# Performance work log

Hardware: AMD Instinct MI355X
Metric: run time of the kernel (lower is better)

Reference implementation:

```python
import jax, jax.numpy as jnp
import numpy as np

N = 20000      # n_nodes
E = 320000     # n_edges (multiple of 4, so _from_coo drops nothing)
D = 512        # embed_dim
H = 8          # num_heads
DK = D // H    # d_k = 64


def setup_inputs() -> dict:
    key = jax.random.key(0)
    ks = jax.random.split(key, 12)
    x = jax.random.normal(ks[0], (N, D), jnp.float32)
    rows = jnp.sort(jax.random.randint(ks[1], (E,), 0, N))
    cols = jax.random.randint(ks[2], (E,), 0, N)
    edge_index = jnp.stack([rows, cols]).astype(jnp.int32)  # [2, E]
    att_bias = jax.random.normal(ks[3], (E, H), jnp.float32)
    s = float(1.0 / np.sqrt(D))  # ~xavier scale
    Wq = jax.random.normal(ks[4], (D, D), jnp.float32) * s
    Wk = jax.random.normal(ks[5], (D, D), jnp.float32) * s
    Wv = jax.random.normal(ks[6], (D, D), jnp.float32) * s
    Wo = jax.random.normal(ks[7], (D, D), jnp.float32) * s
    bq = jnp.zeros((D,), jnp.float32)
    bk = jnp.zeros((D,), jnp.float32)
    bv = jnp.zeros((D,), jnp.float32)
    bo = jnp.zeros((D,), jnp.float32)
    return dict(x=x, edge_index=edge_index, att_bias=att_bias,
                Wq=Wq, bq=bq, Wk=Wk, bk=bk, Wv=Wv, bv=bv, Wo=Wo, bo=bo)


def reference(x, edge_index, att_bias, Wq, bq, Wk, bk, Wv, bv, Wo, bo):
    n = x.shape[0]
    rows, cols = edge_index[0], edge_index[1]
    # per-head projections: [n, H, DK]
    q = (x @ Wq + bq).reshape(n, H, DK)
    k = (x @ Wk + bk).reshape(n, H, DK)
    v = (x @ Wv + bv).reshape(n, H, DK)
    scale = 1.0 / jnp.sqrt(jnp.asarray(DK, x.dtype))
    # masked QK^T on the edge pattern, plus additive bias: [E, H]
    logits = jnp.einsum('ehd,ehd->eh', q[rows] * scale, k[cols]) + att_bias
    # CSR (segment) softmax over each destination row
    row_max = jax.ops.segment_max(logits, rows, num_segments=n)      # [n, H]
    p = jnp.exp(logits - row_max[rows])                              # [E, H]
    denom = jax.ops.segment_sum(p, rows, num_segments=n)            # [n, H]
    att = p / denom[rows]                                            # [E, H]
    # sparse-dense bmm: y[i] = sum_{e: rows[e]=i} att[e] * v[cols[e]]
    y = jax.ops.segment_sum(att[:, :, None] * v[cols], rows, num_segments=n)  # [n, H, DK]
    out = y.reshape(n, H * DK) @ Wo + bo
    return out
```

## Files before the change

kernel.cpp:

```cpp
#include <hip/hip_runtime.h>
#include <hip/hip_bf16.h>

typedef unsigned short ushort_t;
typedef unsigned int uint32;
typedef __attribute__((ext_vector_type(8))) short short8;
typedef __attribute__((ext_vector_type(4))) float floatx4;

#define DEV __device__ __forceinline__

#if defined(__has_builtin)
#if __has_builtin(__builtin_amdgcn_sdot4)
#define HAS_SDOT 1
#endif
#endif
#ifndef HAS_SDOT
#define HAS_SDOT 0
#endif

DEV float b2f(ushort_t u) { return __uint_as_float(((uint32)u) << 16); }
DEV ushort_t f2b(float f) {
  __hip_bfloat16 h = __float2bfloat16(f);
  return __builtin_bit_cast(unsigned short, h);
}
DEV void unpack8(const uint4& u, float* f) {
  f[0] = __uint_as_float(u.x << 16); f[1] = __uint_as_float(u.x & 0xffff0000u);
  f[2] = __uint_as_float(u.y << 16); f[3] = __uint_as_float(u.y & 0xffff0000u);
  f[4] = __uint_as_float(u.z << 16); f[5] = __uint_as_float(u.z & 0xffff0000u);
  f[6] = __uint_as_float(u.w << 16); f[7] = __uint_as_float(u.w & 0xffff0000u);
}
DEV void unpack_i8x8(uint2 u, float* f) {
  f[0] = (float)((int)(u.x << 24) >> 24);
  f[1] = (float)((int)(u.x << 16) >> 24);
  f[2] = (float)((int)(u.x << 8) >> 24);
  f[3] = (float)((int)u.x >> 24);
  f[4] = (float)((int)(u.y << 24) >> 24);
  f[5] = (float)((int)(u.y << 16) >> 24);
  f[6] = (float)((int)(u.y << 8) >> 24);
  f[7] = (float)((int)u.y >> 24);
}

#define GLOAD_LDS(gp, lp) \
  __builtin_amdgcn_global_load_lds((const __attribute__((address_space(1))) uint32*)(gp), \
                                   (__attribute__((address_space(3))) uint32*)(lp), 16, 0, 0)

#define KVROW 1088

__global__ __launch_bounds__(256) void k_detect(const ushort_t* __restrict__ x,
                                                int* __restrict__ flag) {
  __shared__ int red[256];
  int tid = threadIdx.x;
  int wild = 0;
  for (int i = tid; i < 4096; i += 256) {
    uint32 e = (x[i] >> 7) & 0xFFu;
    if (e < 100u || e > 140u) wild++;
  }
  red[tid] = wild;
  __syncthreads();
  for (int s = 128; s > 0; s >>= 1) {
    if (tid < s) red[tid] += red[tid + s];
    __syncthreads();
  }
  if (tid == 0) flag[0] = (red[0] > 400) ? 1 : 0;
}

__global__ __launch_bounds__(256) void k_transpose(
    const void* __restrict__ Wq, const void* __restrict__ Wk,
    const void* __restrict__ Wv, const void* __restrict__ Wo,
    ushort_t* __restrict__ WT4, const int* __restrict__ flagp) {
  __shared__ ushort_t t[32][33];
  int isf32 = *flagp;
  int z = blockIdx.z;
  const void* src = (z == 0) ? Wq : (z == 1) ? Wk : (z == 2) ? Wv : Wo;
  ushort_t* dst = WT4 + (size_t)z * 512 * 512;
  int bx = blockIdx.x, by = blockIdx.y;
  int tx = threadIdx.x, ty = threadIdx.y;
#pragma unroll
  for (int i = 0; i < 4; i++) {
    size_t idx = (size_t)(by * 32 + ty + 8 * i) * 512 + bx * 32 + tx;
    ushort_t v = isf32 ? f2b(((const float*)src)[idx]) : ((const ushort_t*)src)[idx];
    t[ty + 8 * i][tx] = v;
  }
  __syncthreads();
#pragma unroll
  for (int i = 0; i < 4; i++)
    dst[(size_t)(bx * 32 + ty + 8 * i) * 512 + by * 32 + tx] = t[tx][ty + 8 * i];
}

__global__ __launch_bounds__(256) void k_biases(
    const void* __restrict__ bq, const void* __restrict__ bk,
    const void* __restrict__ bv, const void* __restrict__ bo,
    float* __restrict__ biasf, const int* __restrict__ flagp) {
  int i = blockIdx.x * 256 + threadIdx.x;
  if (i >= 2048) return;
  int z = i >> 9, j = i & 511;
  const void* b = (z == 0) ? bq : (z == 1) ? bk : (z == 2) ? bv : bo;
  biasf[i] = (*flagp) ? ((const float*)b)[j] : b2f(((const ushort_t*)b)[j]);
}

__global__ __launch_bounds__(256) void k_convx(
    const void* __restrict__ x, ushort_t* __restrict__ xb, int n8,
    const int* __restrict__ flagp) {
  int i = blockIdx.x * 256 + threadIdx.x;
  if (i >= n8) return;
  if (*flagp) {
    const float* xf = (const float*)x + (size_t)i * 8;
    float4 f0 = ((const float4*)xf)[0];
    float4 f1 = ((const float4*)xf)[1];
    uint4 o;
    o.x = (uint32)f2b(f0.x) | ((uint32)f2b(f0.y) << 16);
    o.y = (uint32)f2b(f0.z) | ((uint32)f2b(f0.w) << 16);
    o.z = (uint32)f2b(f1.x) | ((uint32)f2b(f1.y) << 16);
    o.w = (uint32)f2b(f1.z) | ((uint32)f2b(f1.w) << 16);
    ((uint4*)xb)[i] = o;
  } else {
    ((uint4*)xb)[i] = ((const uint4*)x)[i];
  }
}

__global__ __launch_bounds__(256) void k_convab(
    const void* __restrict__ ab, float* __restrict__ ABc, int n4,
    const int* __restrict__ flagp) {
  if (*flagp) return;
  int i = blockIdx.x * 256 + threadIdx.x;
  if (i >= n4) return;
  uint2 u = ((const uint2*)ab)[i];
  float4 o;
  o.x = __uint_as_float(u.x << 16);
  o.y = __uint_as_float(u.x & 0xffff0000u);
  o.z = __uint_as_float(u.y << 16);
  o.w = __uint_as_float(u.y & 0xffff0000u);
  ((float4*)ABc)[i] = o;
}

__global__ void k_build_rp(const int* __restrict__ rows, int E, int N, int* __restrict__ rp) {
  int i = blockIdx.x * blockDim.x + threadIdx.x;
  if (i > N) return;
  int lo = 0, hi = E;
  while (lo < hi) {
    int mid = (lo + hi) >> 1;
    if (rows[mid] < i) lo = mid + 1; else hi = mid;
  }
  rp[i] = lo;
}

DEV void gemm_body(const ushort_t* __restrict__ A, const ushort_t* __restrict__ BT,
                   const float* __restrict__ bias, void* C,
                   int M, int ldc, float scale, int row0, int by, int mode) {
  __shared__ ushort_t As[2][128 * 32];
  __shared__ ushort_t Bs[2][128 * 32];
  int tid = threadIdx.x;
  int w = tid >> 6, lane = tid & 63;
  int sr = lane >> 2;
  int skz = (((lane & 3) ^ ((lane >> 3) & 3)) * 8);

  floatx4 acc[4][4];
#pragma unroll
  for (int i = 0; i < 4; i++)
#pragma unroll
    for (int j = 0; j < 4; j++)
#pragma unroll
      for (int r = 0; r < 4; r++) acc[i][j][r] = 0.f;

  int lm = lane & 15, quad = lane >> 4;
  int wr = w >> 1, wc = w & 1;
  const int nG = by * 128 + w * 32;

  int rA0 = row0 + w * 32 + sr; if (rA0 >= M) rA0 = M - 1;
  int rA1 = rA0 + 16;          if (rA1 >= M) rA1 = M - 1;
  const ushort_t* gA0 = A + (size_t)rA0 * 512 + skz;
  const ushort_t* gA1 = A + (size_t)rA1 * 512 + skz;
  const ushort_t* gB0 = BT + (size_t)(nG + sr) * 512 + skz;
  const ushort_t* gB1 = BT + (size_t)(nG + 16 + sr) * 512 + skz;

  auto stage = [&](int buf, int k0) {
    GLOAD_LDS(gA0 + k0, &As[buf][(w * 32 + 0) * 32]);
    GLOAD_LDS(gA1 + k0, &As[buf][(w * 32 + 16) * 32]);
    GLOAD_LDS(gB0 + k0, &Bs[buf][(w * 32 + 0) * 32]);
    GLOAD_LDS(gB1 + k0, &Bs[buf][(w * 32 + 16) * 32]);
  };

  int rchunk = (quad ^ ((lm >> 1) & 3)) * 8;

  stage(0, 0);
  __syncthreads();

  for (int ks = 0; ks < 16; ++ks) {
    int cur = ks & 1;
    if (ks < 15) stage(cur ^ 1, (ks + 1) * 32);

    const ushort_t* pa = &As[cur][(wr * 64 + lm) * 32] + rchunk;
    const ushort_t* pb = &Bs[cur][(wc * 64 + lm) * 32] + rchunk;
    short8 af[4], bfr[4];
#pragma unroll
    for (int t4 = 0; t4 < 4; t4++) {
      af[t4]  = *(const short8*)(pa + t4 * 16 * 32);
      bfr[t4] = *(const short8*)(pb + t4 * 16 * 32);
    }
#pragma unroll
    for (int mt = 0; mt < 4; mt++)
#pragma unroll
      for (int nt = 0; nt < 4; nt++)
        acc[mt][nt] = __builtin_amdgcn_mfma_f32_16x16x32_bf16(af[mt], bfr[nt], acc[mt][nt], 0, 0, 0);

    __syncthreads();
  }

  int colB = by * 128 + wc * 64 + lm;
  float bv4[4];
#pragma unroll
  for (int nt = 0; nt < 4; nt++) bv4[nt] = bias[colB + nt * 16];

  if (mode <= 1) {
#pragma unroll
    for (int mt = 0; mt < 4; mt++) {
      int rg0 = row0 + wr * 64 + mt * 16 + quad * 4;
#pragma unroll
      for (int nt = 0; nt < 4; nt++) {
#pragma unroll
        for (int r = 0; r < 4; r++) {
          int rg = rg0 + r;
          if (rg < M) {
            float val = (acc[mt][nt][r] + bv4[nt]) * scale;
            size_t off = (size_t)rg * ldc + colB + nt * 16;
            if (mode == 1) ((float*)C)[off] = val;
            else           ((ushort_t*)C)[off] = f2b(val);
          }
        }
      }
    }
  } else {
    int vslot = (mode == 4);
    int colbase = by * 128 + wc * 64;
    int head = colbase >> 6;
#pragma unroll
    for (int mt = 0; mt < 4; mt++) {
#pragma unroll
      for (int r = 0; r < 4; r++) {
        int rg = row0 + wr * 64 + mt * 16 + quad * 4 + r;
        float v0 = acc[mt][0][r] + bv4[0];
        float v1 = acc[mt][1][r] + bv4[1];
        float v2 = acc[mt][2][r] + bv4[2];
        float v3 = acc[mt][3][r] + bv4[3];
        float am = fmaxf(fmaxf(fabsf(v0), fabsf(v1)), fmaxf(fabsf(v2), fabsf(v3)));
        am = fmaxf(am, __shfl_xor(am, 1));
        am = fmaxf(am, __shfl_xor(am, 2));
        am = fmaxf(am, __shfl_xor(am, 4));
        am = fmaxf(am, __shfl_xor(am, 8));
        am = fmaxf(am, 1e-20f);
        float inv8 = 127.0f / am;
        float sc8 = am * (1.0f / 127.0f);
        if (rg < M) {
          unsigned char* Crow = (unsigned char*)C + (size_t)rg * KVROW;
          unsigned char* bp = Crow + 2 * colbase + 16 * (lm >> 3) + 8 * vslot + (lm & 7);
          bp[ 0] = (unsigned char)(signed char)(int)rintf(v0 * inv8);
          bp[32] = (unsigned char)(signed char)(int)rintf(v1 * inv8);
          bp[64] = (unsigned char)(signed char)(int)rintf(v2 * inv8);
          bp[96] = (unsigned char)(signed char)(int)rintf(v3 * inv8);
          if (lm == 0)
            *(float*)(Crow + 1024 + head * 8 + vslot * 4) = sc8;
        }
      }
    }
  }
}

__global__ __launch_bounds__(256) void k_gemm_qkv(
    const ushort_t* __restrict__ xb, const ushort_t* __restrict__ WT4,
    const float* __restrict__ biasf, ushort_t* Qp, unsigned char* KV8, int M) {
  int z = blockIdx.z;
  const ushort_t* BT = WT4 + (size_t)z * 512 * 512;
  const float* bias = biasf + (size_t)z * 512;
  if (z == 0)
    gemm_body(xb, BT, bias, Qp, M, 512, 0.125f, blockIdx.x * 128, blockIdx.y, 0);
  else
    gemm_body(xb, BT, bias, KV8, M, 0, 1.0f, blockIdx.x * 128, blockIdx.y, z == 1 ? 3 : 4);
}

__global__ __launch_bounds__(256) void k_gemm_out(
    const ushort_t* __restrict__ y, const ushort_t* __restrict__ WT4,
    const float* __restrict__ biasf, void* out, int M,
    const int* __restrict__ flagp) {
  gemm_body(y, WT4 + (size_t)3 * 512 * 512, biasf + 3 * 512, out, M, 512, 1.0f,
            blockIdx.x * 128, blockIdx.y, *flagp);
}

__global__ __launch_bounds__(256) void k_edge(
    ushort_t* Qy, const unsigned char* __restrict__ KV8,
    const void* __restrict__ ab, const float* __restrict__ ABc,
    const int* __restrict__ cols, const int* __restrict__ rp, int Nn,
    const int* __restrict__ flagp) {
  int node = blockIdx.x * 4 + (threadIdx.x >> 6);
  if (node >= Nn) return;
  int lane = threadIdx.x & 63;
  int h8 = lane >> 3;
  const float* abf32 = (*flagp) ? (const float*)ab : ABc;

  uint4 qu = ((const uint4*)(Qy + (size_t)node * 512))[lane];
  float qf[8];
  unpack8(qu, qf);

#if HAS_SDOT
  float qa = 0.f;
#pragma unroll
  for (int j = 0; j < 8; j++) qa = fmaxf(qa, fabsf(qf[j]));
  qa = fmaxf(qa, __shfl_xor(qa, 1));
  qa = fmaxf(qa, __shfl_xor(qa, 2));
  qa = fmaxf(qa, __shfl_xor(qa, 4));
  qa = fmaxf(qa, 1e-20f);
  float qs = qa * (1.0f / 127.0f);
  float qinv = 127.0f / qa;
  int qp0 = 0, qp1 = 0;
#pragma unroll
  for (int j = 0; j < 4; j++) qp0 |= (((int)rintf(qf[j] * qinv)) & 0xFF) << (8 * j);
#pragma unroll
  for (int j = 4; j < 8; j++) qp1 |= (((int)rintf(qf[j] * qinv)) & 0xFF) << (8 * (j - 4));
#endif

  int e0 = rp[node], e1 = rp[node + 1];
  int cnt = e1 - e0;

  float s0 = 0.f, s1 = 0.f;
  float acc0[8], acc1[8];
#pragma unroll
  for (int j = 0; j < 8; j++) { acc0[j] = 0.f; acc1[j] = 0.f; }

  uint4 kvb[4];
  float2 scb[4];
  float abv[4];

  for (int base = 0; base < cnt; base += 64) {
    int rem = cnt - base; if (rem > 64) rem = 64;
    int li = (lane < rem) ? lane : (rem - 1);
    int myc = cols[e0 + base + li];
    const float* abp = abf32 + (size_t)(e0 + base) * 8 + h8;

    auto pref = [&](int t, int slot) {
      int valid = t < rem;
      int c = __builtin_amdgcn_readlane(myc, valid ? t : 0);
      const unsigned char* kvrow = KV8 + (size_t)c * KVROW;
      kvb[slot] = *(const uint4*)(kvrow + lane * 16);
      scb[slot] = *(const float2*)(kvrow + 1024 + h8 * 8);
      float a = abp[(valid ? t : 0) * 8];
      abv[slot] = valid ? a : -1e30f;
    };
    auto consume = [&](int slot, float* acc, float& s) {
#if HAS_SDOT
      int di = __builtin_amdgcn_sdot4(qp0, (int)kvb[slot].x, 0, false);
      di = __builtin_amdgcn_sdot4(qp1, (int)kvb[slot].y, di, false);
      di += __shfl_xor(di, 1);
      di += __shfl_xor(di, 2);
      di += __shfl_xor(di, 4);
      float logit = fminf(fmaf((float)di * qs, scb[slot].x, abv[slot]), 80.f);
#else
      float kf[8];
      uint2 ku; ku.x = kvb[slot].x; ku.y = kvb[slot].y;
      unpack_i8x8(ku, kf);
      float d = 0.f;
#pragma unroll
      for (int j = 0; j < 8; j++) d = fmaf(qf[j], kf[j], d);
      d += __shfl_xor(d, 1);
      d += __shfl_xor(d, 2);
      d += __shfl_xor(d, 4);
      float logit = fminf(fmaf(d, scb[slot].x, abv[slot]), 80.f);
#endif
      float pw = __expf(logit);
      s += pw;
      float pwv = pw * scb[slot].y;
      float vf[8];
      uint2 vu; vu.x = kvb[slot].z; vu.y = kvb[slot].w;
      unpack_i8x8(vu, vf);
#pragma unroll
      for (int j = 0; j < 8; j++) acc[j] = fmaf(pwv, vf[j], acc[j]);
    };

    pref(0, 0); pref(1, 1); pref(2, 2); pref(3, 3);
    int iters = (rem + 3) >> 2;
    for (int it = 0; it < iters; ++it) {
      int nt = it * 4 + 4;
      consume(0, acc0, s0); pref(nt + 0, 0);
      consume(1, acc1, s1); pref(nt + 1, 1);
      consume(2, acc0, s0); pref(nt + 2, 2);
      consume(3, acc1, s1); pref(nt + 3, 3);
    }
  }

  float s = s0 + s1;
  float inv = (cnt > 0 && s > 0.f) ? 1.f / s : 0.f;
  ushort_t hb[8];
#pragma unroll
  for (int j = 0; j < 8; j++) hb[j] = f2b((acc0[j] + acc1[j]) * inv);
  uint4 uh;
  uh.x = (uint32)hb[0] | ((uint32)hb[1] << 16);
  uh.y = (uint32)hb[2] | ((uint32)hb[3] << 16);
  uh.z = (uint32)hb[4] | ((uint32)hb[5] << 16);
  uh.w = (uint32)hb[6] | ((uint32)hb[7] << 16);
  ((uint4*)(Qy + (size_t)node * 512))[lane] = uh;
}

extern "C" void kernel_launch(void* const* d_in, const int* in_sizes, int n_in,
                              void* d_out, int out_size, void* d_ws, size_t ws_size,
                              hipStream_t stream) {
  const void* x  = d_in[0];
  const int* ei  = (const int*)d_in[1];
  const void* ab = d_in[2];
  const void* Wq = d_in[3];
  const void* bq = d_in[4];
  const void* Wk = d_in[5];
  const void* bk = d_in[6];
  const void* Wv = d_in[7];
  const void* bv = d_in[8];
  const void* Wo = d_in[9];
  const void* bo = d_in[10];

  const int D = 512;
  int M = in_sizes[0] / D;
  int E = in_sizes[1] / 2;
  const int* rows = ei;
  const int* cols = ei + E;

  char* p = (char*)d_ws;
  size_t off = 0;
  auto carve = [&](size_t bytes) -> void* {
    off = (off + 255) & ~(size_t)255;
    void* r = p + off;
    off += bytes;
    return r;
  };
  int* flag          = (int*)carve(4);
  ushort_t* WT4      = (ushort_t*)carve((size_t)4 * 512 * 512 * 2);
  float* biasf       = (float*)carve((size_t)4 * 512 * 4);
  ushort_t* xb       = (ushort_t*)carve((size_t)M * 512 * 2);
  ushort_t* Qp       = (ushort_t*)carve((size_t)M * 512 * 2);
  unsigned char* KV8 = (unsigned char*)carve((size_t)M * KVROW);
  int* rp            = (int*)carve((size_t)(M + 1) * 4);
  (void)ws_size;
  float* ABc = (float*)xb;

  k_detect<<<1, 256, 0, stream>>>((const ushort_t*)x, flag);
  k_transpose<<<dim3(16, 16, 4), dim3(32, 8), 0, stream>>>(Wq, Wk, Wv, Wo, WT4, flag);
  k_biases<<<8, 256, 0, stream>>>(bq, bk, bv, bo, biasf, flag);
  int n8 = M * 512 / 8;
  k_convx<<<(n8 + 255) / 256, 256, 0, stream>>>(x, xb, n8, flag);
  k_build_rp<<<(M + 1 + 255) / 256, 256, 0, stream>>>(rows, E, M, rp);

  int rb = (M + 127) / 128;
  k_gemm_qkv<<<dim3(rb, 4, 3), 256, 0, stream>>>(xb, WT4, biasf, Qp, KV8, M);
  int n4 = E * 8 / 4;
  k_convab<<<(n4 + 255) / 256, 256, 0, stream>>>(ab, ABc, n4, flag);
  k_edge<<<(M + 3) / 4, 256, 0, stream>>>(Qp, KV8, ab, ABc, cols, rp, M, flag);
  k_gemm_out<<<dim3(rb, 4, 1), 256, 0, stream>>>(Qp, WT4, biasf, d_out, M, flag);
}
```

Measured before the change: 274.8 us.

## Pipeline GEMM K-loop with explicit waitcnt barriers and XCD-aware block swizzle

Restructures the GEMM K-loop so the next tile's global-to-LDS load is issued before waiting, using partial vmcnt waits and raw s_barrier instead of __syncthreads, and peels the final iteration. Both GEMM launches are flattened to 1D grids with an XCD-aware remap, so blocks sharing the same row of x/y land on the same chiplet and its L2. The aim is to overlap memory with MFMA work and improve L2 reuse. The hand-written waitcnt counts assume exactly four outstanding loads per stage, which is fragile if the compiler reorders memory operations.

```diff
diff --git a/kernel.cpp b/kernel.cpp
--- a/kernel.cpp
+++ b/kernel.cpp
@@ -44,6 +44,12 @@
                                    (__attribute__((address_space(3))) uint32*)(lp), 16, 0, 0)
 
 #define KVROW 1088
+
+DEV int xcd_swz(int wg, int nwg) {
+  int q = nwg >> 3, r = nwg & 7;
+  int xcd = wg & 7, idx = wg >> 3;
+  return (xcd < r ? xcd * (q + 1) : r * (q + 1) + (xcd - r) * q) + idx;
+}
 
 __global__ __launch_bounds__(256) void k_detect(const ushort_t* __restrict__ x,
                                                 int* __restrict__ flag) {
@@ -181,13 +187,7 @@
 
   int rchunk = (quad ^ ((lm >> 1) & 3)) * 8;
 
-  stage(0, 0);
-  __syncthreads();
-
-  for (int ks = 0; ks < 16; ++ks) {
-    int cur = ks & 1;
-    if (ks < 15) stage(cur ^ 1, (ks + 1) * 32);
-
+  auto compute = [&](int cur) {
     const ushort_t* pa = &As[cur][(wr * 64 + lm) * 32] + rchunk;
     const ushort_t* pb = &Bs[cur][(wc * 64 + lm) * 32] + rchunk;
     short8 af[4], bfr[4];
@@ -201,9 +201,21 @@
 #pragma unroll
       for (int nt = 0; nt < 4; nt++)
         acc[mt][nt] = __builtin_amdgcn_mfma_f32_16x16x32_bf16(af[mt], bfr[nt], acc[mt][nt], 0, 0, 0);
-
-    __syncthreads();
-  }
+  };
+
+  stage(0, 0);
+  for (int ks = 0; ks < 15; ++ks) {
+    int cur = ks & 1;
+    stage(cur ^ 1, (ks + 1) * 32);
+    asm volatile("s_waitcnt vmcnt(4)" ::: "memory");
+    __builtin_amdgcn_s_barrier();
+    compute(cur);
+    asm volatile("s_waitcnt lgkmcnt(0)" ::: "memory");
+    __builtin_amdgcn_s_barrier();
+  }
+  asm volatile("s_waitcnt vmcnt(0)" ::: "memory");
+  __builtin_amdgcn_s_barrier();
+  compute(1);
 
   int colB = by * 128 + wc * 64 + lm;
   float bv4[4];
@@ -267,21 +279,26 @@
 __global__ __launch_bounds__(256) void k_gemm_qkv(
     const ushort_t* __restrict__ xb, const ushort_t* __restrict__ WT4,
     const float* __restrict__ biasf, ushort_t* Qp, unsigned char* KV8, int M) {
-  int z = blockIdx.z;
+  int swz = xcd_swz(blockIdx.x, gridDim.x);
+  int row = swz / 12;
+  int sub = swz - row * 12;
+  int by = sub & 3, z = sub >> 2;
   const ushort_t* BT = WT4 + (size_t)z * 512 * 512;
   const float* bias = biasf + (size_t)z * 512;
   if (z == 0)
-    gemm_body(xb, BT, bias, Qp, M, 512, 0.125f, blockIdx.x * 128, blockIdx.y, 0);
+    gemm_body(xb, BT, bias, Qp, M, 512, 0.125f, row * 128, by, 0);
   else
-    gemm_body(xb, BT, bias, KV8, M, 0, 1.0f, blockIdx.x * 128, blockIdx.y, z == 1 ? 3 : 4);
+    gemm_body(xb, BT, bias, KV8, M, 0, 1.0f, row * 128, by, z == 1 ? 3 : 4);
 }
 
 __global__ __launch_bounds__(256) void k_gemm_out(
     const ushort_t* __restrict__ y, const ushort_t* __restrict__ WT4,
     const float* __restrict__ biasf, void* out, int M,
     const int* __restrict__ flagp) {
+  int swz = xcd_swz(blockIdx.x, gridDim.x);
+  int row = swz >> 2, by = swz & 3;
   gemm_body(y, WT4 + (size_t)3 * 512 * 512, biasf + 3 * 512, out, M, 512, 1.0f,
-            blockIdx.x * 128, blockIdx.y, *flagp);
+            row * 128, by, *flagp);
 }
 
 __global__ __launch_bounds__(256) void k_edge(
@@ -444,9 +461,9 @@
   k_build_rp<<<(M + 1 + 255) / 256, 256, 0, stream>>>(rows, E, M, rp);
 
   int rb = (M + 127) / 128;
-  k_gemm_qkv<<<dim3(rb, 4, 3), 256, 0, stream>>>(xb, WT4, biasf, Qp, KV8, M);
+  k_gemm_qkv<<<rb * 12, 256, 0, stream>>>(xb, WT4, biasf, Qp, KV8, M);
   int n4 = E * 8 / 4;
   k_convab<<<(n4 + 255) / 256, 256, 0, stream>>>(ab, ABc, n4, flag);
   k_edge<<<(M + 3) / 4, 256, 0, stream>>>(Qp, KV8, ab, ABc, cols, rp, M, flag);
-  k_gemm_out<<<dim3(rb, 4, 1), 256, 0, stream>>>(Qp, WT4, biasf, d_out, M, flag);
-}
+  k_gemm_out<<<rb * 4, 256, 0, stream>>>(Qp, WT4, biasf, d_out, M, flag);
+}
```

Measured after the change: 268.7 us. 2.2% less time.
